# Performance work log

Hardware: AMD Instinct MI355X
Metric: run time of the kernel (lower is better)

The kernel has to match this reference:

```python
import jax, jax.numpy as jnp
import numpy as np

B, S, HID = 2, 1024, 2048
NH, NKV = 32, 8
HD = HID // NH          # 64
N_REP = NH // NKV       # 4
ROPE_BASE = 10000.0


def rope_tables(seq_len, dim):
    inv_freq = 1.0 / (ROPE_BASE ** (np.arange(0, dim, 2, dtype=np.float32) / dim))
    t = jnp.arange(seq_len, dtype=jnp.float32)
    freqs = jnp.outer(t, jnp.asarray(inv_freq))          # [S, HD/2]
    emb = jnp.concatenate([freqs, freqs], axis=-1)       # [S, HD]
    return jnp.cos(emb), jnp.sin(emb)


def rotate_half(x):
    half = x.shape[-1] // 2
    return jnp.concatenate([-x[..., half:], x[..., :half]], axis=-1)


def setup_inputs() -> dict:
    key = jax.random.key(0)
    k1, k2, k3, k4, k5 = jax.random.split(key, 5)
    hidden_states = jax.random.normal(k1, (B, S, HID), dtype=jnp.float32)
    position_ids = jnp.broadcast_to(jnp.arange(S, dtype=jnp.int32), (B, S))
    # additive causal mask [B,1,S,S]: 0 where allowed, large negative where masked
    neg = jnp.finfo(jnp.float32).min
    causal = jnp.tril(jnp.ones((S, S), dtype=bool))
    attention_mask = jnp.where(causal, 0.0, neg)[None, None].astype(jnp.float32)
    attention_mask = jnp.broadcast_to(attention_mask, (B, 1, S, S))
    scale = 0.02
    Wq = jax.random.normal(k2, (HID, NH * HD), dtype=jnp.float32) * scale
    Wk = jax.random.normal(k3, (HID, NKV * HD), dtype=jnp.float32) * scale
    Wv = jax.random.normal(k4, (HID, NKV * HD), dtype=jnp.float32) * scale
    Wo = jax.random.normal(k5, (HID, HID), dtype=jnp.float32) * scale
    return {"hidden_states": hidden_states, "position_ids": position_ids,
            "attention_mask": attention_mask, "Wq": Wq, "Wk": Wk, "Wv": Wv, "Wo": Wo}


def reference(hidden_states, position_ids, attention_mask, Wq, Wk, Wv, Wo):
    b, s, _ = hidden_states.shape
    q = (hidden_states @ Wq).reshape(b, s, NH, HD).transpose(0, 2, 1, 3)    # [b,H,s,d]
    k = (hidden_states @ Wk).reshape(b, s, NKV, HD).transpose(0, 2, 1, 3)   # [b,kv,s,d]
    v = (hidden_states @ Wv).reshape(b, s, NKV, HD).transpose(0, 2, 1, 3)

    cos_t, sin_t = rope_tables(s, HD)                    # [s, d]
    cos = cos_t[position_ids][:, None]                   # [b,1,s,d]
    sin = sin_t[position_ids][:, None]
    q = q * cos + rotate_half(q) * sin
    k = k * cos + rotate_half(k) * sin

    # GQA: repeat each kv head N_REP times along the head axis
    k = jnp.repeat(k, N_REP, axis=1)                     # [b,H,s,d]
    v = jnp.repeat(v, N_REP, axis=1)

    scale = 1.0 / jnp.sqrt(jnp.asarray(HD, dtype=q.dtype))
    scores = jnp.einsum('bhqd,bhkd->bhqk', q, k) * scale
    scores = scores + attention_mask
    scores = jnp.maximum(scores, jnp.finfo(scores.dtype).min)
    w = jax.nn.softmax(scores, axis=-1)
    out = jnp.einsum('bhqk,bhkd->bhqd', w, v)            # [b,H,s,d]
    out = out.transpose(0, 2, 1, 3).reshape(b, s, HID)
    return out @ Wo
```

## Files before the change

### kernel.cpp

```cpp
#include <hip/hip_runtime.h>
#include <hip/hip_bf16.h>
#include <math.h>

constexpr int BB   = 2;
constexpr int SS   = 1024;
constexpr int HID  = 2048;
constexpr int NH   = 32;
constexpr int NKV  = 8;
constexpr int HD   = 64;
constexpr int M    = BB * SS;
constexpr int NQKV = 3072;

typedef __attribute__((ext_vector_type(8))) short bf8v;
typedef __attribute__((ext_vector_type(4))) float f4v;

static __device__ __forceinline__ unsigned short f2b(float x) {
  __hip_bfloat16 h = __float2bfloat16(x);
  return *reinterpret_cast<unsigned short*>(&h);
}
static __device__ __forceinline__ float b2f(unsigned short u) {
  return __uint_as_float(((unsigned)u) << 16);
}
static __device__ __forceinline__ void gload16(void* lds, const void* g) {
  __builtin_amdgcn_global_load_lds(
      (const __attribute__((address_space(1))) void*)g,
      (__attribute__((address_space(3))) void*)lds, 16, 0, 0);
}

__global__ __launch_bounds__(256) void castX(const float* __restrict__ src,
                                             unsigned short* __restrict__ dst) {
  const size_t i = ((size_t)blockIdx.x * 256 + threadIdx.x) * 8;
  const float4 v0 = *(const float4*)(src + i);
  const float4 v1 = *(const float4*)(src + i + 4);
  unsigned short o[8] = {f2b(v0.x), f2b(v0.y), f2b(v0.z), f2b(v0.w),
                         f2b(v1.x), f2b(v1.y), f2b(v1.z), f2b(v1.w)};
  *(bf8v*)(dst + i) = *(bf8v*)o;
}

__global__ __launch_bounds__(256) void wtrans(const float* __restrict__ src,
                                              unsigned short* __restrict__ dst,
                                              int R, int C) {
  const int r0 = blockIdx.y * 64, c0 = blockIdx.x * 64;
  __shared__ float T[64][65];
  const int t = threadIdx.x;
  {
    const int r  = t >> 2;
    const int c4 = (t & 3) * 16;
    const float* sp = src + (size_t)(r0 + r) * C + c0 + c4;
    *(float4*)&T[r][c4 + 0]  = *(const float4*)(sp + 0);
    *(float4*)&T[r][c4 + 4]  = *(const float4*)(sp + 4);
    *(float4*)&T[r][c4 + 8]  = *(const float4*)(sp + 8);
    *(float4*)&T[r][c4 + 12] = *(const float4*)(sp + 12);
  }
  __syncthreads();
  {
    const int c  = t >> 2;
    const int rr = (t & 3) * 16;
    unsigned short o[16];
#pragma unroll
    for (int i = 0; i < 16; ++i) o[i] = f2b(T[rr + i][c]);
    unsigned short* dp = dst + (size_t)(c0 + c) * R + r0 + rr;
    *(bf8v*)dp       = *(bf8v*)&o[0];
    *(bf8v*)(dp + 8) = *(bf8v*)&o[8];
  }
}

__global__ __launch_bounds__(256) void gemm_bf16(
    const unsigned short* __restrict__ A, const unsigned short* __restrict__ Bt,
    void* __restrict__ Cout, int Ndim, int Kdim, int outBf16) {
  __shared__ unsigned short As[2][128 * 32];
  __shared__ unsigned short Bs[2][128 * 32];
  const int t  = threadIdx.x;
  const int w  = t >> 6, l = t & 63;
  const int lr = l & 15, lg = l >> 4;
  const int wr = w >> 1, wc = w & 1;
  const int bm = blockIdx.y * 128, bn = blockIdx.x * 128;

  f4v acc[4][4] = {};

  const unsigned short* Ablk = A  + (size_t)bm * Kdim;
  const unsigned short* Bblk = Bt + (size_t)bn * Kdim;
  const int srow = l >> 2;
  const int scol = (l & 3) * 8;

  auto stage = [&](int buf, int k0) {
    gload16(&As[buf][(w * 32)      * 32], Ablk + (size_t)(w * 32 +      srow) * Kdim + k0 + scol);
    gload16(&As[buf][(w * 32 + 16) * 32], Ablk + (size_t)(w * 32 + 16 + srow) * Kdim + k0 + scol);
    gload16(&Bs[buf][(w * 32)      * 32], Bblk + (size_t)(w * 32 +      srow) * Kdim + k0 + scol);
    gload16(&Bs[buf][(w * 32 + 16) * 32], Bblk + (size_t)(w * 32 + 16 + srow) * Kdim + k0 + scol);
  };

  stage(0, 0);
  __syncthreads();
  int cur = 0;
  for (int k0 = 0; k0 < Kdim; k0 += 32) {
    if (k0 + 32 < Kdim) stage(cur ^ 1, k0 + 32);

    bf8v aF[4], bF[4];
#pragma unroll
    for (int i = 0; i < 4; ++i) {
      aF[i] = *(const bf8v*)&As[cur][(wr * 64 + i * 16 + lr) * 32 + lg * 8];
      bF[i] = *(const bf8v*)&Bs[cur][(wc * 64 + i * 16 + lr) * 32 + lg * 8];
    }
    __builtin_amdgcn_s_setprio(1);
#pragma unroll
    for (int mi = 0; mi < 4; ++mi)
#pragma unroll
      for (int ni = 0; ni < 4; ++ni)
        acc[mi][ni] = __builtin_amdgcn_mfma_f32_16x16x32_bf16(aF[mi], bF[ni], acc[mi][ni], 0, 0, 0);
    __builtin_amdgcn_s_setprio(0);

    __syncthreads();
    cur ^= 1;
  }

  const int row0 = bm + wr * 64;
  const int col0 = bn + wc * 64;
  if (outBf16) {
    unsigned short* C = (unsigned short*)Cout;
#pragma unroll
    for (int mi = 0; mi < 4; ++mi)
#pragma unroll
      for (int r = 0; r < 4; ++r) {
        const size_t rowoff = (size_t)(row0 + mi * 16 + lg * 4 + r) * Ndim;
#pragma unroll
        for (int ni = 0; ni < 4; ++ni)
          C[rowoff + col0 + ni * 16 + lr] = f2b(acc[mi][ni][r]);
      }
  } else {
    float* C = (float*)Cout;
#pragma unroll
    for (int mi = 0; mi < 4; ++mi)
#pragma unroll
      for (int r = 0; r < 4; ++r) {
        const size_t rowoff = (size_t)(row0 + mi * 16 + lg * 4 + r) * Ndim;
#pragma unroll
        for (int ni = 0; ni < 4; ++ni)
          C[rowoff + col0 + ni * 16 + lr] = acc[mi][ni][r];
      }
  }
}

__global__ __launch_bounds__(256) void rope_qk(
    const unsigned short* __restrict__ qkv, const int* __restrict__ pos_ids,
    unsigned short* __restrict__ Qb, unsigned short* __restrict__ Kb) {
  const int m = blockIdx.x;
  const int b = m >> 10;
  const int s = m & (SS - 1);
  const int t = threadIdx.x;
  __shared__ float cst[32], snt[32];
  if (t < 32) {
    const float pos = (float)pos_ids[m];
    const float ang = pos * exp2f(-(float)t * (13.287712379549449f / 32.0f));
    float sn, cs;
    sincosf(ang, &sn, &cs);
    cst[t] = cs;
    snt[t] = sn;
  }
  __syncthreads();
  const unsigned short* row = qkv + (size_t)m * NQKV;
  for (int i = t; i < HID; i += 256) {
    const int h = i >> 6, d = i & 63, j = d & 31;
    const float x   = b2f(row[i]);
    const float prt = b2f(row[h * 64 + ((d < 32) ? d + 32 : d - 32)]);
    const float rh  = (d < 32) ? -prt : prt;
    Qb[((size_t)((b * NH + h) * SS + s)) * 64 + d] = f2b((x * cst[j] + rh * snt[j]) * 0.125f);
  }
  for (int i = t; i < NKV * HD; i += 256) {
    const int h = i >> 6, d = i & 63, j = d & 31;
    const float x   = b2f(row[2048 + i]);
    const float prt = b2f(row[2048 + h * 64 + ((d < 32) ? d + 32 : d - 32)]);
    const float rh  = (d < 32) ? -prt : prt;
    Kb[((size_t)((b * NKV + h) * SS + s)) * 64 + d] = f2b(x * cst[j] + rh * snt[j]);
  }
}

__global__ __launch_bounds__(256) void vtrans2(
    const unsigned short* __restrict__ qkv, unsigned short* __restrict__ Vt) {
  const int bkv = blockIdx.y;
  const int b = bkv >> 3, kv = bkv & 7;
  const int s0 = blockIdx.x * 64;
  __shared__ unsigned short T[64][72];
  const int t = threadIdx.x;
  const unsigned short* src = qkv + (size_t)(b * SS + s0) * NQKV + 2560 + kv * 64;
  {
    const int r  = t >> 2;
    const int co = (t & 3) * 16;
    *(bf8v*)&T[r][co]     = *(const bf8v*)(src + (size_t)r * NQKV + co);
    *(bf8v*)&T[r][co + 8] = *(const bf8v*)(src + (size_t)r * NQKV + co + 8);
  }
  __syncthreads();
  {
    const int d  = t >> 2;
    const int so = (t & 3) * 16;
    unsigned short tmp[16];
#pragma unroll
    for (int i = 0; i < 16; ++i) tmp[i] = T[so + i][d];
    unsigned short* dst = Vt + ((size_t)(bkv * 64 + d)) * SS + s0 + so;
    *(bf8v*)dst       = *(bf8v*)&tmp[0];
    *(bf8v*)(dst + 8) = *(bf8v*)&tmp[8];
  }
}

__global__ __launch_bounds__(128) void attn_mfma(
    const unsigned short* __restrict__ Qb, const unsigned short* __restrict__ Kb,
    const unsigned short* __restrict__ Vt, unsigned short* __restrict__ attn) {
  const int xb = blockIdx.x;
  const int h = blockIdx.y, b = blockIdx.z;
  const int kv = h >> 2;
  const int w  = threadIdx.x >> 6;
  const int l  = threadIdx.x & 63;
  const int lr = l & 15;
  const int lg = l >> 4;
  const int t  = threadIdx.x;

  __shared__ unsigned short VT[64][72];
  __shared__ unsigned short PL[2][16][72];

  const unsigned short* Kp = Kb + ((size_t)((b * NKV + kv) * SS)) * 64;
  const unsigned short* Vp = Vt + ((size_t)((b * NKV + kv) * 64)) * SS;

  const int vd  = t >> 1;
  const int vso = (t & 1) * 32;

  for (int half = 0; half < 2; ++half) {
    const int qt = half ? (31 - xb) : xb;
    const int qbase = qt * 32;
    const int qW = qbase + w * 16;
    const unsigned short* Qp = Qb + ((size_t)((b * NH + h) * SS + qW)) * 64;
    bf8v aQ0 = *(const bf8v*)(Qp + (size_t)lr * 64 + lg * 8);
    bf8v aQ1 = *(const bf8v*)(Qp + (size_t)lr * 64 + 32 + lg * 8);

    f4v o[4] = {{0,0,0,0},{0,0,0,0},{0,0,0,0},{0,0,0,0}};
    float lsumL[4] = {0.f, 0.f, 0.f, 0.f};

    for (int kvb = 0; kvb < qbase + 32; kvb += 64) {
      __syncthreads();
      const unsigned short* vp = Vp + (size_t)vd * SS + kvb + vso;
      const bf8v v0 = *(const bf8v*)(vp);
      const bf8v v1 = *(const bf8v*)(vp + 8);
      const bf8v v2 = *(const bf8v*)(vp + 16);
      const bf8v v3 = *(const bf8v*)(vp + 24);

      f4v sc[4] = {{0,0,0,0},{0,0,0,0},{0,0,0,0},{0,0,0,0}};
      __builtin_amdgcn_s_setprio(1);
#pragma unroll
      for (int c = 0; c < 4; ++c) {
        const unsigned short* kr = Kp + (size_t)(kvb + c * 16 + lr) * 64 + lg * 8;
        bf8v b0 = *(const bf8v*)(kr);
        bf8v b1 = *(const bf8v*)(kr + 32);
        sc[c] = __builtin_amdgcn_mfma_f32_16x16x32_bf16(aQ0, b0, sc[c], 0, 0, 0);
        sc[c] = __builtin_amdgcn_mfma_f32_16x16x32_bf16(aQ1, b1, sc[c], 0, 0, 0);
      }
      __builtin_amdgcn_s_setprio(0);

#pragma unroll
      for (int r = 0; r < 4; ++r) {
        const int qrow = qW + lg * 4 + r;
        float ps = 0.f;
        unsigned short pb[4];
#pragma unroll
        for (int c = 0; c < 4; ++c) {
          const float s = ((kvb + c * 16 + lr) > qrow) ? -INFINITY : sc[c][r];
          const float p = __expf(s);
          ps += p;
          pb[c] = f2b(p);
        }
        lsumL[r] += ps;
#pragma unroll
        for (int c = 0; c < 4; ++c) PL[w][lg * 4 + r][c * 16 + lr] = pb[c];
      }

      *(bf8v*)&VT[vd][vso]      = v0;
      *(bf8v*)&VT[vd][vso + 8]  = v1;
      *(bf8v*)&VT[vd][vso + 16] = v2;
      *(bf8v*)&VT[vd][vso + 24] = v3;

      __syncthreads();

      bf8v aP0 = *(const bf8v*)&PL[w][lr][lg * 8];
      bf8v aP1 = *(const bf8v*)&PL[w][lr][32 + lg * 8];
      __builtin_amdgcn_s_setprio(1);
#pragma unroll
      for (int n = 0; n < 4; ++n) {
        bf8v bV0 = *(const bf8v*)&VT[n * 16 + lr][lg * 8];
        bf8v bV1 = *(const bf8v*)&VT[n * 16 + lr][32 + lg * 8];
        o[n] = __builtin_amdgcn_mfma_f32_16x16x32_bf16(aP0, bV0, o[n], 0, 0, 0);
        o[n] = __builtin_amdgcn_mfma_f32_16x16x32_bf16(aP1, bV1, o[n], 0, 0, 0);
      }
      __builtin_amdgcn_s_setprio(0);
    }

#pragma unroll
    for (int r = 0; r < 4; ++r) {
      float ls = lsumL[r];
      ls += __shfl_xor(ls, 1);
      ls += __shfl_xor(ls, 2);
      ls += __shfl_xor(ls, 4);
      ls += __shfl_xor(ls, 8);
      const float inv = 1.0f / ls;
      const int row = qW + lg * 4 + r;
      unsigned short* dst = attn + (size_t)(b * SS + row) * HID + h * 64;
#pragma unroll
      for (int n = 0; n < 4; ++n) dst[n * 16 + lr] = f2b(o[n][r] * inv);
    }
  }
}

extern "C" void kernel_launch(void* const* d_in, const int* in_sizes, int n_in,
                              void* d_out, int out_size, void* d_ws, size_t ws_size,
                              hipStream_t stream) {
  const float* hidden = (const float*)d_in[0];
  const int*   pos    = (const int*)d_in[1];
  const float* Wq = (const float*)d_in[3];
  const float* Wk = (const float*)d_in[4];
  const float* Wv = (const float*)d_in[5];
  const float* Wo = (const float*)d_in[6];
  float* out = (float*)d_out;

  char* ws = (char*)d_ws;
  unsigned short* WqkvT = (unsigned short*)(ws);
  unsigned short* WoT   = (unsigned short*)(ws + 12582912);
  unsigned short* Xb    = (unsigned short*)(ws + 20971520);
  unsigned short* qkvr  = (unsigned short*)(ws + 29360128);
  unsigned short* Qb    = (unsigned short*)(ws + 20971520);
  unsigned short* attnb = (unsigned short*)(ws + 29360128);
  unsigned short* Kb    = (unsigned short*)(ws + 41943040);
  unsigned short* Vt    = (unsigned short*)(ws + 44040192);

  dim3 blk(256);

  castX<<<dim3(M * HID / 2048), blk, 0, stream>>>(hidden, Xb);
  wtrans<<<dim3(32, 32), blk, 0, stream>>>(Wq, WqkvT, HID, HID);
  wtrans<<<dim3(8, 32),  blk, 0, stream>>>(Wk, WqkvT + (size_t)2048 * HID, HID, 512);
  wtrans<<<dim3(8, 32),  blk, 0, stream>>>(Wv, WqkvT + (size_t)2560 * HID, HID, 512);
  wtrans<<<dim3(32, 32), blk, 0, stream>>>(Wo, WoT, HID, HID);

  gemm_bf16<<<dim3(NQKV / 128, M / 128), blk, 0, stream>>>(Xb, WqkvT, qkvr, NQKV, HID, 1);

  rope_qk<<<dim3(M), blk, 0, stream>>>(qkvr, pos, Qb, Kb);
  vtrans2<<<dim3(SS / 64, BB * NKV), blk, 0, stream>>>(qkvr, Vt);

  attn_mfma<<<dim3(16, NH, BB), dim3(128), 0, stream>>>(Qb, Kb, Vt, attnb);

  gemm_bf16<<<dim3(HID / 128, M / 128), blk, 0, stream>>>(attnb, WoT, out, HID, HID, 0);
}
```

Before: 157.5 us.

## Merge weight transposes into one launch and halve GEMM tile rows

New measurement: 161.7 us. +2.7%, slower.

```diff
diff --git a/kernel.cpp b/kernel.cpp
--- a/kernel.cpp
+++ b/kernel.cpp
@@ -37,10 +37,21 @@
   *(bf8v*)(dst + i) = *(bf8v*)o;
 }
 
-__global__ __launch_bounds__(256) void wtrans(const float* __restrict__ src,
-                                              unsigned short* __restrict__ dst,
-                                              int R, int C) {
+__global__ __launch_bounds__(256) void wtransAll(
+    const float* __restrict__ Wq, const float* __restrict__ Wk,
+    const float* __restrict__ Wv, const float* __restrict__ Wo,
+    unsigned short* __restrict__ WqkvT, unsigned short* __restrict__ WoT) {
+  const int z = blockIdx.z;
+  const float* src;
+  unsigned short* dst;
+  int C;
+  if (z == 0)      { src = Wq; dst = WqkvT;                        C = 2048; }
+  else if (z == 1) { src = Wk; dst = WqkvT + (size_t)2048 * HID;   C = 512;  }
+  else if (z == 2) { src = Wv; dst = WqkvT + (size_t)2560 * HID;   C = 512;  }
+  else             { src = Wo; dst = WoT;                          C = 2048; }
+
   const int r0 = blockIdx.y * 64, c0 = blockIdx.x * 64;
+  if (c0 >= C) return;
   __shared__ float T[64][65];
   const int t = threadIdx.x;
   {
@@ -59,7 +70,7 @@
     unsigned short o[16];
 #pragma unroll
     for (int i = 0; i < 16; ++i) o[i] = f2b(T[rr + i][c]);
-    unsigned short* dp = dst + (size_t)(c0 + c) * R + r0 + rr;
+    unsigned short* dp = dst + (size_t)(c0 + c) * HID + r0 + rr;
     *(bf8v*)dp       = *(bf8v*)&o[0];
     *(bf8v*)(dp + 8) = *(bf8v*)&o[8];
   }
@@ -68,15 +79,15 @@
 __global__ __launch_bounds__(256) void gemm_bf16(
     const unsigned short* __restrict__ A, const unsigned short* __restrict__ Bt,
     void* __restrict__ Cout, int Ndim, int Kdim, int outBf16) {
-  __shared__ unsigned short As[2][128 * 32];
+  __shared__ unsigned short As[2][64 * 32];
   __shared__ unsigned short Bs[2][128 * 32];
   const int t  = threadIdx.x;
   const int w  = t >> 6, l = t & 63;
   const int lr = l & 15, lg = l >> 4;
   const int wr = w >> 1, wc = w & 1;
-  const int bm = blockIdx.y * 128, bn = blockIdx.x * 128;
-
-  f4v acc[4][4] = {};
+  const int bm = blockIdx.y * 64, bn = blockIdx.x * 128;
+
+  f4v acc[2][4] = {};
 
   const unsigned short* Ablk = A  + (size_t)bm * Kdim;
   const unsigned short* Bblk = Bt + (size_t)bn * Kdim;
@@ -84,8 +95,7 @@
   const int scol = (l & 3) * 8;
 
   auto stage = [&](int buf, int k0) {
-    gload16(&As[buf][(w * 32)      * 32], Ablk + (size_t)(w * 32 +      srow) * Kdim + k0 + scol);
-    gload16(&As[buf][(w * 32 + 16) * 32], Ablk + (size_t)(w * 32 + 16 + srow) * Kdim + k0 + scol);
+    gload16(&As[buf][(w * 16) * 32], Ablk + (size_t)(w * 16 + srow) * Kdim + k0 + scol);
     gload16(&Bs[buf][(w * 32)      * 32], Bblk + (size_t)(w * 32 +      srow) * Kdim + k0 + scol);
     gload16(&Bs[buf][(w * 32 + 16) * 32], Bblk + (size_t)(w * 32 + 16 + srow) * Kdim + k0 + scol);
   };
@@ -96,15 +106,16 @@
   for (int k0 = 0; k0 < Kdim; k0 += 32) {
     if (k0 + 32 < Kdim) stage(cur ^ 1, k0 + 32);
 
-    bf8v aF[4], bF[4];
-#pragma unroll
-    for (int i = 0; i < 4; ++i) {
-      aF[i] = *(const bf8v*)&As[cur][(wr * 64 + i * 16 + lr) * 32 + lg * 8];
-      bF[i] = *(const bf8v*)&Bs[cur][(wc * 64 + i * 16 + lr) * 32 + lg * 8];
-    }
+    bf8v aF[2], bF[4];
+#pragma unroll
+    for (int i = 0; i < 2; ++i)
+      aF[i] = *(const bf8v*)&As[cur][(wr * 32 + i * 16 + lr) * 32 + lg * 8];
+#pragma unroll
+    for (int j = 0; j < 4; ++j)
+      bF[j] = *(const bf8v*)&Bs[cur][(wc * 64 + j * 16 + lr) * 32 + lg * 8];
     __builtin_amdgcn_s_setprio(1);
 #pragma unroll
-    for (int mi = 0; mi < 4; ++mi)
+    for (int mi = 0; mi < 2; ++mi)
 #pragma unroll
       for (int ni = 0; ni < 4; ++ni)
         acc[mi][ni] = __builtin_amdgcn_mfma_f32_16x16x32_bf16(aF[mi], bF[ni], acc[mi][ni], 0, 0, 0);
@@ -114,12 +125,12 @@
     cur ^= 1;
   }
 
-  const int row0 = bm + wr * 64;
+  const int row0 = bm + wr * 32;
   const int col0 = bn + wc * 64;
   if (outBf16) {
     unsigned short* C = (unsigned short*)Cout;
 #pragma unroll
-    for (int mi = 0; mi < 4; ++mi)
+    for (int mi = 0; mi < 2; ++mi)
 #pragma unroll
       for (int r = 0; r < 4; ++r) {
         const size_t rowoff = (size_t)(row0 + mi * 16 + lg * 4 + r) * Ndim;
@@ -130,7 +141,7 @@
   } else {
     float* C = (float*)Cout;
 #pragma unroll
-    for (int mi = 0; mi < 4; ++mi)
+    for (int mi = 0; mi < 2; ++mi)
 #pragma unroll
       for (int r = 0; r < 4; ++r) {
         const size_t rowoff = (size_t)(row0 + mi * 16 + lg * 4 + r) * Ndim;
@@ -331,17 +342,14 @@
   dim3 blk(256);
 
   castX<<<dim3(M * HID / 2048), blk, 0, stream>>>(hidden, Xb);
-  wtrans<<<dim3(32, 32), blk, 0, stream>>>(Wq, WqkvT, HID, HID);
-  wtrans<<<dim3(8, 32),  blk, 0, stream>>>(Wk, WqkvT + (size_t)2048 * HID, HID, 512);
-  wtrans<<<dim3(8, 32),  blk, 0, stream>>>(Wv, WqkvT + (size_t)2560 * HID, HID, 512);
-  wtrans<<<dim3(32, 32), blk, 0, stream>>>(Wo, WoT, HID, HID);
-
-  gemm_bf16<<<dim3(NQKV / 128, M / 128), blk, 0, stream>>>(Xb, WqkvT, qkvr, NQKV, HID, 1);
+  wtransAll<<<dim3(32, 32, 4), blk, 0, stream>>>(Wq, Wk, Wv, Wo, WqkvT, WoT);
+
+  gemm_bf16<<<dim3(NQKV / 128, M / 64), blk, 0, stream>>>(Xb, WqkvT, qkvr, NQKV, HID, 1);
 
   rope_qk<<<dim3(M), blk, 0, stream>>>(qkvr, pos, Qb, Kb);
   vtrans2<<<dim3(SS / 64, BB * NKV), blk, 0, stream>>>(qkvr, Vt);
 
   attn_mfma<<<dim3(16, NH, BB), dim3(128), 0, stream>>>(Qb, Kb, Vt, attnb);
 
-  gemm_bf16<<<dim3(HID / 128, M / 128), blk, 0, stream>>>(attnb, WoT, out, HID, HID, 0);
-}
+  gemm_bf16<<<dim3(HID / 128, M / 64), blk, 0, stream>>>(attnb, WoT, out, HID, HID, 0);
+}
```

## Fuse RoPE into QKV GEMM epilogue and merge prep kernels into one launch

Applied to the files above, without the earlier changes.

After: 162.8 us. +3.4%, slower.

```diff
diff --git a/kernel.cpp b/kernel.cpp
--- a/kernel.cpp
+++ b/kernel.cpp
@@ -18,31 +18,59 @@
   __hip_bfloat16 h = __float2bfloat16(x);
   return *reinterpret_cast<unsigned short*>(&h);
 }
-static __device__ __forceinline__ float b2f(unsigned short u) {
-  return __uint_as_float(((unsigned)u) << 16);
-}
 static __device__ __forceinline__ void gload16(void* lds, const void* g) {
   __builtin_amdgcn_global_load_lds(
       (const __attribute__((address_space(1))) void*)g,
       (__attribute__((address_space(3))) void*)lds, 16, 0, 0);
 }
 
-__global__ __launch_bounds__(256) void castX(const float* __restrict__ src,
-                                             unsigned short* __restrict__ dst) {
-  const size_t i = ((size_t)blockIdx.x * 256 + threadIdx.x) * 8;
-  const float4 v0 = *(const float4*)(src + i);
-  const float4 v1 = *(const float4*)(src + i + 4);
-  unsigned short o[8] = {f2b(v0.x), f2b(v0.y), f2b(v0.z), f2b(v0.w),
-                         f2b(v1.x), f2b(v1.y), f2b(v1.z), f2b(v1.w)};
-  *(bf8v*)(dst + i) = *(bf8v*)o;
-}
-
-__global__ __launch_bounds__(256) void wtrans(const float* __restrict__ src,
-                                              unsigned short* __restrict__ dst,
-                                              int R, int C) {
+__global__ __launch_bounds__(256) void prepAll(
+    const float* __restrict__ Wq, const float* __restrict__ Wk,
+    const float* __restrict__ Wv, const float* __restrict__ Wo,
+    const float* __restrict__ hidden, const int* __restrict__ pos_ids,
+    unsigned short* __restrict__ WqkvT, unsigned short* __restrict__ WoT,
+    unsigned short* __restrict__ Xb, float2* __restrict__ tab) {
+  const int z = blockIdx.z;
+  const int t = threadIdx.x;
+
+  if (z == 4) {
+    const int idx = blockIdx.y * 32 + blockIdx.x;
+    if ((t & 127) < 32) {
+      const int m = idx * 2 + (t >> 7);
+      const int j = t & 31;
+      const float pos = (float)pos_ids[m];
+      const float ang = pos * exp2f(-(float)j * (13.287712379549449f / 32.0f));
+      float sn, cs;
+      sincosf(ang, &sn, &cs);
+      tab[(size_t)m * 32 + j] = make_float2(cs, sn);
+    }
+    return;
+  }
+  if (z == 5) {
+    const size_t base = ((size_t)(blockIdx.y * 32 + blockIdx.x)) * 4096;
+#pragma unroll
+    for (int it = 0; it < 2; ++it) {
+      const size_t i = base + it * 2048 + t * 8;
+      const float4 v0 = *(const float4*)(hidden + i);
+      const float4 v1 = *(const float4*)(hidden + i + 4);
+      unsigned short o[8] = {f2b(v0.x), f2b(v0.y), f2b(v0.z), f2b(v0.w),
+                             f2b(v1.x), f2b(v1.y), f2b(v1.z), f2b(v1.w)};
+      *(bf8v*)(Xb + i) = *(bf8v*)o;
+    }
+    return;
+  }
+
+  const float* src;
+  unsigned short* dst;
+  int C;
+  if (z == 0)      { src = Wq; dst = WqkvT;                      C = 2048; }
+  else if (z == 1) { src = Wk; dst = WqkvT + (size_t)2048 * HID; C = 512;  }
+  else if (z == 2) { src = Wv; dst = WqkvT + (size_t)2560 * HID; C = 512;  }
+  else             { src = Wo; dst = WoT;                        C = 2048; }
+
   const int r0 = blockIdx.y * 64, c0 = blockIdx.x * 64;
+  if (c0 >= C) return;
   __shared__ float T[64][65];
-  const int t = threadIdx.x;
   {
     const int r  = t >> 2;
     const int c4 = (t & 3) * 16;
@@ -59,15 +87,104 @@
     unsigned short o[16];
 #pragma unroll
     for (int i = 0; i < 16; ++i) o[i] = f2b(T[rr + i][c]);
-    unsigned short* dp = dst + (size_t)(c0 + c) * R + r0 + rr;
+    unsigned short* dp = dst + (size_t)(c0 + c) * HID + r0 + rr;
     *(bf8v*)dp       = *(bf8v*)&o[0];
     *(bf8v*)(dp + 8) = *(bf8v*)&o[8];
   }
 }
 
+__global__ __launch_bounds__(256) void gemm_qkv(
+    const unsigned short* __restrict__ A, const unsigned short* __restrict__ Bt,
+    const float2* __restrict__ tab,
+    unsigned short* __restrict__ Qb, unsigned short* __restrict__ Kb,
+    unsigned short* __restrict__ Vb) {
+  __shared__ unsigned short As[2][128 * 32];
+  __shared__ unsigned short Bs[2][128 * 32];
+  const int Kdim = HID;
+  const int t  = threadIdx.x;
+  const int w  = t >> 6, l = t & 63;
+  const int lr = l & 15, lg = l >> 4;
+  const int wr = w >> 1, wc = w & 1;
+  const int bm = blockIdx.y * 128, bn = blockIdx.x * 128;
+
+  f4v acc[4][4] = {};
+
+  const unsigned short* Ablk = A  + (size_t)bm * Kdim;
+  const unsigned short* Bblk = Bt + (size_t)bn * Kdim;
+  const int srow = l >> 2;
+  const int scol = (l & 3) * 8;
+
+  auto stage = [&](int buf, int k0) {
+    gload16(&As[buf][(w * 32)      * 32], Ablk + (size_t)(w * 32 +      srow) * Kdim + k0 + scol);
+    gload16(&As[buf][(w * 32 + 16) * 32], Ablk + (size_t)(w * 32 + 16 + srow) * Kdim + k0 + scol);
+    gload16(&Bs[buf][(w * 32)      * 32], Bblk + (size_t)(w * 32 +      srow) * Kdim + k0 + scol);
+    gload16(&Bs[buf][(w * 32 + 16) * 32], Bblk + (size_t)(w * 32 + 16 + srow) * Kdim + k0 + scol);
+  };
+
+  stage(0, 0);
+  __syncthreads();
+  int cur = 0;
+  for (int k0 = 0; k0 < Kdim; k0 += 32) {
+    if (k0 + 32 < Kdim) stage(cur ^ 1, k0 + 32);
+
+    bf8v aF[4], bF[4];
+#pragma unroll
+    for (int i = 0; i < 4; ++i) {
+      aF[i] = *(const bf8v*)&As[cur][(wr * 64 + i * 16 + lr) * 32 + lg * 8];
+      bF[i] = *(const bf8v*)&Bs[cur][(wc * 64 + i * 16 + lr) * 32 + lg * 8];
+    }
+    __builtin_amdgcn_s_setprio(1);
+#pragma unroll
+    for (int mi = 0; mi < 4; ++mi)
+#pragma unroll
+      for (int ni = 0; ni < 4; ++ni)
+        acc[mi][ni] = __builtin_amdgcn_mfma_f32_16x16x32_bf16(aF[mi], bF[ni], acc[mi][ni], 0, 0, 0);
+    __builtin_amdgcn_s_setprio(0);
+
+    __syncthreads();
+    cur ^= 1;
+  }
+
+  const int row0 = bm + wr * 64;
+  const int colHead = bn + wc * 64;
+  unsigned short* outArr;
+  int hh, headsPerB, mode;
+  if (colHead < 2048)      { mode = 0; outArr = Qb; hh = colHead >> 6;          headsPerB = NH;  }
+  else if (colHead < 2560) { mode = 1; outArr = Kb; hh = (colHead - 2048) >> 6; headsPerB = NKV; }
+  else                     { mode = 2; outArr = Vb; hh = (colHead - 2560) >> 6; headsPerB = NKV; }
+
+#pragma unroll
+  for (int mi = 0; mi < 4; ++mi)
+#pragma unroll
+    for (int r = 0; r < 4; ++r) {
+      const int rowg = row0 + mi * 16 + lg * 4 + r;
+      const int bI = rowg >> 10, s = rowg & (SS - 1);
+      unsigned short* dst =
+          outArr + ((size_t)(bI * headsPerB + hh) * SS + s) * 64;
+      if (mode == 2) {
+#pragma unroll
+        for (int ni = 0; ni < 4; ++ni)
+          dst[ni * 16 + lr] = f2b(acc[mi][ni][r]);
+      } else {
+        const float2 cs_lo = tab[(size_t)rowg * 32 + lr];
+        const float2 cs_hi = tab[(size_t)rowg * 32 + 16 + lr];
+#pragma unroll
+        for (int ni = 0; ni < 4; ++ni) {
+          const float2 cs = (ni & 1) ? cs_hi : cs_lo;
+          const float x   = acc[mi][ni][r];
+          const float prt = acc[mi][ni ^ 2][r];
+          const float rh  = (ni < 2) ? -prt : prt;
+          float v = x * cs.x + rh * cs.y;
+          if (mode == 0) v *= 0.125f;
+          dst[ni * 16 + lr] = f2b(v);
+        }
+      }
+    }
+}
+
 __global__ __launch_bounds__(256) void gemm_bf16(
     const unsigned short* __restrict__ A, const unsigned short* __restrict__ Bt,
-    void* __restrict__ Cout, int Ndim, int Kdim, int outBf16) {
+    float* __restrict__ C, int Ndim, int Kdim) {
   __shared__ unsigned short As[2][128 * 32];
   __shared__ unsigned short Bs[2][128 * 32];
   const int t  = threadIdx.x;
@@ -116,78 +233,29 @@
 
   const int row0 = bm + wr * 64;
   const int col0 = bn + wc * 64;
-  if (outBf16) {
-    unsigned short* C = (unsigned short*)Cout;
-#pragma unroll
-    for (int mi = 0; mi < 4; ++mi)
-#pragma unroll
-      for (int r = 0; r < 4; ++r) {
-        const size_t rowoff = (size_t)(row0 + mi * 16 + lg * 4 + r) * Ndim;
-#pragma unroll
-        for (int ni = 0; ni < 4; ++ni)
-          C[rowoff + col0 + ni * 16 + lr] = f2b(acc[mi][ni][r]);
-      }
-  } else {
-    float* C = (float*)Cout;
-#pragma unroll
-    for (int mi = 0; mi < 4; ++mi)
-#pragma unroll
-      for (int r = 0; r < 4; ++r) {
-        const size_t rowoff = (size_t)(row0 + mi * 16 + lg * 4 + r) * Ndim;
-#pragma unroll
-        for (int ni = 0; ni < 4; ++ni)
-          C[rowoff + col0 + ni * 16 + lr] = acc[mi][ni][r];
-      }
-  }
-}
-
-__global__ __launch_bounds__(256) void rope_qk(
-    const unsigned short* __restrict__ qkv, const int* __restrict__ pos_ids,
-    unsigned short* __restrict__ Qb, unsigned short* __restrict__ Kb) {
-  const int m = blockIdx.x;
-  const int b = m >> 10;
-  const int s = m & (SS - 1);
-  const int t = threadIdx.x;
-  __shared__ float cst[32], snt[32];
-  if (t < 32) {
-    const float pos = (float)pos_ids[m];
-    const float ang = pos * exp2f(-(float)t * (13.287712379549449f / 32.0f));
-    float sn, cs;
-    sincosf(ang, &sn, &cs);
-    cst[t] = cs;
-    snt[t] = sn;
-  }
-  __syncthreads();
-  const unsigned short* row = qkv + (size_t)m * NQKV;
-  for (int i = t; i < HID; i += 256) {
-    const int h = i >> 6, d = i & 63, j = d & 31;
-    const float x   = b2f(row[i]);
-    const float prt = b2f(row[h * 64 + ((d < 32) ? d + 32 : d - 32)]);
-    const float rh  = (d < 32) ? -prt : prt;
-    Qb[((size_t)((b * NH + h) * SS + s)) * 64 + d] = f2b((x * cst[j] + rh * snt[j]) * 0.125f);
-  }
-  for (int i = t; i < NKV * HD; i += 256) {
-    const int h = i >> 6, d = i & 63, j = d & 31;
-    const float x   = b2f(row[2048 + i]);
-    const float prt = b2f(row[2048 + h * 64 + ((d < 32) ? d + 32 : d - 32)]);
-    const float rh  = (d < 32) ? -prt : prt;
-    Kb[((size_t)((b * NKV + h) * SS + s)) * 64 + d] = f2b(x * cst[j] + rh * snt[j]);
-  }
-}
-
-__global__ __launch_bounds__(256) void vtrans2(
-    const unsigned short* __restrict__ qkv, unsigned short* __restrict__ Vt) {
+#pragma unroll
+  for (int mi = 0; mi < 4; ++mi)
+#pragma unroll
+    for (int r = 0; r < 4; ++r) {
+      const size_t rowoff = (size_t)(row0 + mi * 16 + lg * 4 + r) * Ndim;
+#pragma unroll
+      for (int ni = 0; ni < 4; ++ni)
+        C[rowoff + col0 + ni * 16 + lr] = acc[mi][ni][r];
+    }
+}
+
+__global__ __launch_bounds__(256) void vtrans(
+    const unsigned short* __restrict__ Vb, unsigned short* __restrict__ Vt) {
   const int bkv = blockIdx.y;
-  const int b = bkv >> 3, kv = bkv & 7;
-  const int s0 = blockIdx.x * 64;
+  const int s0  = blockIdx.x * 64;
   __shared__ unsigned short T[64][72];
   const int t = threadIdx.x;
-  const unsigned short* src = qkv + (size_t)(b * SS + s0) * NQKV + 2560 + kv * 64;
+  const unsigned short* src = Vb + ((size_t)bkv * SS + s0) * 64;
   {
     const int r  = t >> 2;
     const int co = (t & 3) * 16;
-    *(bf8v*)&T[r][co]     = *(const bf8v*)(src + (size_t)r * NQKV + co);
-    *(bf8v*)&T[r][co + 8] = *(const bf8v*)(src + (size_t)r * NQKV + co + 8);
+    *(bf8v*)&T[r][co]     = *(const bf8v*)(src + (size_t)r * 64 + co);
+    *(bf8v*)&T[r][co + 8] = *(const bf8v*)(src + (size_t)r * 64 + co + 8);
   }
   __syncthreads();
   {
@@ -322,26 +390,23 @@
   unsigned short* WqkvT = (unsigned short*)(ws);
   unsigned short* WoT   = (unsigned short*)(ws + 12582912);
   unsigned short* Xb    = (unsigned short*)(ws + 20971520);
-  unsigned short* qkvr  = (unsigned short*)(ws + 29360128);
-  unsigned short* Qb    = (unsigned short*)(ws + 20971520);
-  unsigned short* attnb = (unsigned short*)(ws + 29360128);
-  unsigned short* Kb    = (unsigned short*)(ws + 41943040);
-  unsigned short* Vt    = (unsigned short*)(ws + 44040192);
+  unsigned short* attnb = Xb;
+  unsigned short* Qb    = (unsigned short*)(ws + 29360128);
+  unsigned short* Kb    = (unsigned short*)(ws + 37748736);
+  unsigned short* Vb    = (unsigned short*)(ws + 39845888);
+  unsigned short* Vt    = (unsigned short*)(ws + 41943040);
+  float2*         tab   = (float2*)(ws + 44040192);
 
   dim3 blk(256);
 
-  castX<<<dim3(M * HID / 2048), blk, 0, stream>>>(hidden, Xb);
-  wtrans<<<dim3(32, 32), blk, 0, stream>>>(Wq, WqkvT, HID, HID);
-  wtrans<<<dim3(8, 32),  blk, 0, stream>>>(Wk, WqkvT + (size_t)2048 * HID, HID, 512);
-  wtrans<<<dim3(8, 32),  blk, 0, stream>>>(Wv, WqkvT + (size_t)2560 * HID, HID, 512);
-  wtrans<<<dim3(32, 32), blk, 0, stream>>>(Wo, WoT, HID, HID);
-
-  gemm_bf16<<<dim3(NQKV / 128, M / 128), blk, 0, stream>>>(Xb, WqkvT, qkvr, NQKV, HID, 1);
-
-  rope_qk<<<dim3(M), blk, 0, stream>>>(qkvr, pos, Qb, Kb);
-  vtrans2<<<dim3(SS / 64, BB * NKV), blk, 0, stream>>>(qkvr, Vt);
+  prepAll<<<dim3(32, 32, 6), blk, 0, stream>>>(Wq, Wk, Wv, Wo, hidden, pos,
+                                               WqkvT, WoT, Xb, tab);
+
+  gemm_qkv<<<dim3(NQKV / 128, M / 128), blk, 0, stream>>>(Xb, WqkvT, tab, Qb, Kb, Vb);
+
+  vtrans<<<dim3(SS / 64, BB * NKV), blk, 0, stream>>>(Vb, Vt);
 
   attn_mfma<<<dim3(16, NH, BB), dim3(128), 0, stream>>>(Qb, Kb, Vt, attnb);
 
-  gemm_bf16<<<dim3(HID / 128, M / 128), blk, 0, stream>>>(attnb, WoT, out, HID, HID, 0);
-}
+  gemm_bf16<<<dim3(HID / 128, M / 128), blk, 0, stream>>>(attnb, WoT, out, HID, HID);
+}
```
